# Optimization experiments

Measured on AMD Instinct MI355X. Metric: run time of the kernel, lower is better.

The kernel has to match this reference:

```python
import jax, jax.numpy as jnp
import numpy as np

B, C_IN, C_HID, H, W = 4, 512, 512, 64, 64


def setup_inputs() -> dict:
    key = jax.random.key(0)
    ks = jax.random.split(key, 9)
    s_in = 1.0 / np.sqrt(C_IN)
    s_hid = 1.0 / np.sqrt(C_HID)
    return {
        "inp": jax.random.normal(ks[0], (B, C_IN, H, W), dtype=jnp.float32),
        "Wk": jax.random.normal(ks[1], (C_HID, C_IN), dtype=jnp.float32) * s_in,
        "bk": jax.random.normal(ks[2], (C_HID,), dtype=jnp.float32) * 0.01,
        "Wq": jax.random.normal(ks[3], (C_HID, C_IN), dtype=jnp.float32) * s_in,
        "bq": jax.random.normal(ks[4], (C_HID,), dtype=jnp.float32) * 0.01,
        "Wv": jax.random.normal(ks[5], (C_HID, C_IN), dtype=jnp.float32) * s_in,
        "bv": jax.random.normal(ks[6], (C_HID,), dtype=jnp.float32) * 0.01,
        "Wo": jax.random.normal(ks[7], (C_IN, C_HID), dtype=jnp.float32) * s_hid,
        "bo": jax.random.normal(ks[8], (C_IN,), dtype=jnp.float32) * 0.01,
    }


def reference(inp, Wk, bk, Wq, bq, Wv, bv, Wo, bo):
    b, _, h, w = inp.shape
    n = h * w

    def conv1x1(x, Wt, bias):  # 1x1 conv == per-pixel GEMM
        return jnp.einsum('bchw,oc->bohw', x, Wt) + bias[None, :, None, None]

    k = conv1x1(inp, Wk, bk).reshape(b, C_HID, n)   # [B,Ch,N]
    q = conv1x1(inp, Wq, bq).reshape(b, C_HID, n)
    v = conv1x1(inp, Wv, bv).reshape(b, C_HID, n)

    scale = 1.0 / jnp.sqrt(jnp.asarray(C_HID, dtype=jnp.float32))
    # weight[b,i,j] = <key_i, query_j> / sqrt(Ch); softmax over j (dim=2)
    scores = jnp.einsum('bci,bcj->bij', k, q) * scale  # [B,N,N]
    weight = jax.nn.softmax(scores, axis=2)
    # out[b,c,i] = sum_j weight[b,i,j] * v[b,c,j]
    out = jnp.einsum('bij,bcj->bci', weight, v).reshape(b, C_HID, h, w)
    return conv1x1(out, Wo, bo)  # [B,C_in,H,W]
```

## Files before the change

### kernel.cpp

```cpp
#include <hip/hip_runtime.h>
#include <hip/hip_bf16.h>


typedef __attribute__((ext_vector_type(4))) float f32x4;
typedef __attribute__((ext_vector_type(8))) short short8;
typedef __attribute__((ext_vector_type(4))) short short4v;

#define QSCALE 0.06376639774f

__device__ __forceinline__ unsigned short f2bf(float f) {
  unsigned u = __builtin_bit_cast(unsigned, f);
  unsigned r = (u + 0x7FFFu + ((u >> 16) & 1u)) >> 16;
  return (unsigned short)r;
}

__device__ __forceinline__ void gll16(const void* g, void* l) {
  __builtin_amdgcn_global_load_lds((const __attribute__((address_space(1))) void*)g,
                                   (__attribute__((address_space(3))) void*)l, 16, 0, 0);
}

#define MFMA_BF16(d, va, vb) \
  d = __builtin_amdgcn_mfma_f32_16x16x32_bf16(va, vb, d, 0, 0, 0)

__device__ __forceinline__ void gemm_fat(
    const short* __restrict__ A, int lda,
    const short* __restrict__ B, int ldb,
    int nkt, char* sm, f32x4 (&acc)[8][4]) {
  const int tid = threadIdx.x, w = tid >> 6, lane = tid & 63;
  const int g = lane >> 4, l15 = lane & 15;
  const int swz = (l15 & 7) << 4;

  for (int t = 0; t < nkt; ++t) {
    __syncthreads();
#pragma unroll
    for (int reg = 0; reg < 3; ++reg) {
      const short* src = reg ? B : A;
      const int ld = reg ? ldb : lda;
      const int rbase = (reg == 2) ? 128 : 0;
#pragma unroll
      for (int pass = 0; pass < 4; ++pass) {
        int chunk = pass * 4 + w;
        int o = chunk * 1024 + lane * 16;
        int row = o >> 7;
        int cb = (o & 127) ^ ((row & 7) << 4);
        gll16((const char*)src + (size_t)(rbase + row) * (ld * 2) +
                  (size_t)t * 128 + cb,
              sm + reg * 16384 + chunk * 1024);
      }
    }
    __syncthreads();
#pragma unroll
    for (int ks = 0; ks < 2; ++ks) {
      short8 a[8], bb[4];
#pragma unroll
      for (int i = 0; i < 8; ++i)
        a[i] = *(const short8*)(sm + (i * 16 + l15) * 128 + ((ks * 64 + g * 16) ^ swz));
#pragma unroll
      for (int nf = 0; nf < 4; ++nf) {
        int r = w * 64 + nf * 16 + l15;
        bb[nf] = *(const short8*)(sm + 16384 + (r >> 7) * 16384 + (r & 127) * 128 +
                                  ((ks * 64 + g * 16) ^ swz));
      }
      __builtin_amdgcn_s_setprio(1);
#pragma unroll
      for (int i = 0; i < 8; ++i)
#pragma unroll
        for (int nf = 0; nf < 4; ++nf)
          MFMA_BF16(acc[i][nf], a[i], bb[nf]);
      __builtin_amdgcn_s_setprio(0);
    }
  }
}

__global__ __launch_bounds__(256) void cvt_w_kernel(
    const float* __restrict__ wk, const float* __restrict__ wq,
    const float* __restrict__ wv, const float* __restrict__ wo,
    short* __restrict__ o) {
  int z = blockIdx.y;
  const float* s = (z == 0) ? wk : (z == 1) ? wq : (z == 2) ? wv : wo;
  int i = blockIdx.x * 256 + threadIdx.x;
  float4 f = ((const float4*)s)[i];
  short4v v;
  v[0] = (short)f2bf(f.x); v[1] = (short)f2bf(f.y);
  v[2] = (short)f2bf(f.z); v[3] = (short)f2bf(f.w);
  if (z < 3) {
    *(short4v*)(o + z * 262144 + i * 4) = v;
  } else {
    int idx = i * 4, co = idx >> 9, cc = idx & 511;
    short* base = o + 786432 + co * 1024 + cc;
    *(short4v*)base = v;
    *(short4v*)(base + 512) = v;
  }
}

__global__ __launch_bounds__(256) void transpose_x_kernel(
    const float* __restrict__ inp, short* __restrict__ xt) {
  __shared__ float t[32][33];
  int tx = threadIdx.x, ty = threadIdx.y;
  int n0 = blockIdx.x * 32, c0 = blockIdx.y * 32, b = blockIdx.z;
  const float* src = inp + ((size_t)(b * 512 + c0)) * 4096 + n0;
#pragma unroll
  for (int r = 0; r < 4; ++r) t[ty + r * 8][tx] = src[(ty + r * 8) * 4096 + tx];
  __syncthreads();
  short* dst = xt + ((size_t)((b << 12) + n0)) * 512 + c0;
#pragma unroll
  for (int r = 0; r < 4; ++r) dst[(ty + r * 8) * 512 + tx] = (short)f2bf(t[tx][ty + r * 8]);
}

__global__ __launch_bounds__(256, 2) void kqv_kernel(
    const short* __restrict__ xt,
    const short* __restrict__ wk, const short* __restrict__ wq, const short* __restrict__ wv,
    const float* __restrict__ bk, const float* __restrict__ bq, const float* __restrict__ bv,
    short* __restrict__ kt, short* __restrict__ qt, short* __restrict__ vc) {
  __shared__ char sm[49152];
  const int bid = blockIdx.x;
  const int xcd = bid & 7, s = bid >> 3;
  const int gg = (s / 12) * 8 + xcd;
  const int t = s % 12;
  const int z = (t < 8) ? (t >> 2) : 2;
  const short *A, *B;
  int arow0, brow0;
  if (z < 2) {
    arow0 = gg * 256 + ((t >> 1) & 1) * 128;
    brow0 = (t & 1) * 256;
    A = xt + (size_t)arow0 * 512;
    B = ((z == 0) ? wk : wq) + (size_t)brow0 * 512;
  } else {
    arow0 = (t - 8) * 128;
    brow0 = gg * 256;
    A = wv + (size_t)arow0 * 512;
    B = xt + (size_t)brow0 * 512;
  }
  f32x4 acc[8][4] = {};
  gemm_fat(A, 512, B, 512, 8, sm, acc);
  const int tid = threadIdx.x, w = tid >> 6, lane = tid & 63;
  const int gq = lane >> 4, l15 = lane & 15;
#pragma unroll
  for (int mf = 0; mf < 8; ++mf)
#pragma unroll
    for (int nf = 0; nf < 4; ++nf)
#pragma unroll
      for (int r = 0; r < 4; ++r) {
        int row = mf * 16 + gq * 4 + r;
        int col = w * 64 + nf * 16 + l15;
        float v = acc[mf][nf][r];
        if (z == 0)      kt[(size_t)(arow0 + row) * 512 + brow0 + col] =
                           (short)f2bf((v + bk[brow0 + col]) * QSCALE);
        else if (z == 1) qt[(size_t)(arow0 + row) * 512 + brow0 + col] =
                           (short)f2bf(v + bq[brow0 + col]);
        else             vc[(size_t)(arow0 + row) * 16384 + brow0 + col] =
                           (short)f2bf(v + bv[arow0 + row]);
      }
}

__global__ __launch_bounds__(256, 2) void gemm_s_kernel(
    const short* __restrict__ kt, const short* __restrict__ qt,
    short* __restrict__ P, float* __restrict__ Lpart) {
  __shared__ char sm[49152];
  const int bid = blockIdx.x;
  const int xcd = bid & 7, s = bid >> 3;
  const int b = xcd >> 1, h = xcd & 1;
  const int it = s >> 3, jt = s & 7;
  const int i0 = it * 128, jt0 = jt * 256;
  const short* A = kt + ((size_t)((b << 12) + i0)) * 512;
  const short* B = qt + ((size_t)((b << 12) + h * 2048 + jt0)) * 512;
  f32x4 acc[8][4] = {};
  gemm_fat(A, 512, B, 512, 8, sm, acc);
  const int tid = threadIdx.x, w = tid >> 6, lane = tid & 63;
  const int gq = lane >> 4, l15 = lane & 15;
  short* Pb = P + (size_t)h * 33554432 + ((size_t)((b << 12) + i0)) * 2048 + jt0;
  float psum[8][4];
#pragma unroll
  for (int mf = 0; mf < 8; ++mf)
#pragma unroll
    for (int r = 0; r < 4; ++r) psum[mf][r] = 0.f;
#pragma unroll
  for (int mf = 0; mf < 8; ++mf)
#pragma unroll
    for (int nf = 0; nf < 4; ++nf)
#pragma unroll
      for (int r = 0; r < 4; ++r) {
        float p = exp2f(acc[mf][nf][r]);
        psum[mf][r] += p;
        int row = mf * 16 + gq * 4 + r;
        int col = w * 64 + nf * 16 + l15;
        Pb[(size_t)row * 2048 + col] = (short)f2bf(p);
      }
  const int jp = (h * 2048 + jt0 + w * 64) >> 6;
  float* Lp = Lpart + (((size_t)b * 64 + jp) << 12) + i0;
#pragma unroll
  for (int mf = 0; mf < 8; ++mf)
#pragma unroll
    for (int r = 0; r < 4; ++r) {
      float ss = psum[mf][r];
      ss += __shfl_xor(ss, 1); ss += __shfl_xor(ss, 2);
      ss += __shfl_xor(ss, 4); ss += __shfl_xor(ss, 8);
      if (l15 == 0) Lp[mf * 16 + gq * 4 + r] = ss;
    }
}

__global__ __launch_bounds__(256, 2) void gemm_pv_kernel(
    const short* __restrict__ P, const short* __restrict__ vc,
    short* __restrict__ otab) {
  __shared__ char sm[49152];
  const int bid = blockIdx.x;
  const int xcd = bid & 7, s = bid >> 3;
  const int b = xcd >> 1, h = xcd & 1;
  const int it = s >> 1, ct = s & 1;
  const int i0 = it * 128, c0 = ct * 256;
  const short* A = P + (size_t)h * 33554432 + ((size_t)((b << 12) + i0)) * 2048;
  const short* B = vc + (size_t)c0 * 16384 + (b << 12) + h * 2048;
  f32x4 acc[8][4] = {};
  gemm_fat(A, 2048, B, 16384, 32, sm, acc);
  const int tid = threadIdx.x, w = tid >> 6, lane = tid & 63;
  const int gq = lane >> 4, l15 = lane & 15;
  short* Ob = otab + ((size_t)((b << 12) + i0)) * 1024 + h * 512 + c0;
#pragma unroll
  for (int mf = 0; mf < 8; ++mf)
#pragma unroll
    for (int nf = 0; nf < 4; ++nf)
#pragma unroll
      for (int r = 0; r < 4; ++r) {
        int row = mf * 16 + gq * 4 + r;
        int col = w * 64 + nf * 16 + l15;
        Ob[(size_t)row * 1024 + col] = (short)f2bf(acc[mf][nf][r]);
      }
}

__global__ __launch_bounds__(256) void lred_kernel(
    const float* __restrict__ Lpart, float* __restrict__ linv) {
  int i = blockIdx.x * 256 + threadIdx.x;
  int b = i >> 12;
  float s = 0.f;
#pragma unroll 8
  for (int jp = 0; jp < 64; ++jp) s += Lpart[(((size_t)b * 64 + jp) << 12) + (i & 4095)];
  linv[i] = 1.0f / s;
}

__global__ __launch_bounds__(256, 2) void gemm_out_kernel(
    const short* __restrict__ wdup, const short* __restrict__ otab,
    const float* __restrict__ bo, const float* __restrict__ linv,
    float* __restrict__ out) {
  __shared__ char sm[49152];
  const int bid = blockIdx.x;
  const int xcd = bid & 7, s = bid >> 3;
  const int b = xcd >> 1, ch = xcd & 1;
  const int cot = ch * 2 + (s & 1);
  const int nt = s >> 1;
  const int arow0 = cot * 128;
  const int bn0 = nt * 256;
  const short* A = wdup + (size_t)arow0 * 1024;
  const short* B = otab + ((size_t)((b << 12) + bn0)) * 1024;
  f32x4 acc[8][4] = {};
  gemm_fat(A, 1024, B, 1024, 16, sm, acc);
  const int tid = threadIdx.x, w = tid >> 6, lane = tid & 63;
  const int gq = lane >> 4, l15 = lane & 15;
#pragma unroll
  for (int mf = 0; mf < 8; ++mf) {
    int co = arow0 + mf * 16 + gq * 4;
#pragma unroll
    for (int nf = 0; nf < 4; ++nf) {
      int nl = bn0 + w * 64 + nf * 16 + l15;
      float li = linv[(b << 12) + nl];
#pragma unroll
      for (int r = 0; r < 4; ++r)
        out[((size_t)(b * 512 + co + r) << 12) + nl] = acc[mf][nf][r] * li + bo[co + r];
    }
  }
}

extern "C" void kernel_launch(void* const* d_in, const int* in_sizes, int n_in,
                              void* d_out, int out_size, void* d_ws, size_t ws_size,
                              hipStream_t stream) {
  const float* inp = (const float*)d_in[0];
  const float* Wk = (const float*)d_in[1];
  const float* bk = (const float*)d_in[2];
  const float* Wq = (const float*)d_in[3];
  const float* bq = (const float*)d_in[4];
  const float* Wv = (const float*)d_in[5];
  const float* bv = (const float*)d_in[6];
  const float* Wo = (const float*)d_in[7];
  const float* bo = (const float*)d_in[8];
  float* out = (float*)d_out;
  char* ws = (char*)d_ws;
  const size_t MB = 1048576;
  short* kt    = (short*)(ws);
  short* qt    = (short*)(ws + 16 * MB);
  short* vc    = (short*)(ws + 32 * MB);
  short* wb    = (short*)(ws + 48 * MB);
  short* xt    = (short*)(ws + 51 * MB);
  float* Lpart = (float*)(ws + 51 * MB);
  float* linv  = (float*)(ws + 55 * MB);
  short* P     = (short*)(ws + 67 * MB);
  short* otab  = (short*)(ws + 195 * MB);

  (void)in_sizes; (void)n_in; (void)out_size; (void)ws_size;

  cvt_w_kernel<<<dim3(256, 4), 256, 0, stream>>>(Wk, Wq, Wv, Wo, wb);
  transpose_x_kernel<<<dim3(128, 16, 4), dim3(32, 8, 1), 0, stream>>>(inp, xt);
  kqv_kernel<<<768, 256, 0, stream>>>(
      xt, wb, wb + 262144, wb + 524288, bk, bq, bv, kt, qt, vc);
  gemm_s_kernel<<<2048, 256, 0, stream>>>(kt, qt, P, Lpart);
  gemm_pv_kernel<<<512, 256, 0, stream>>>(P, vc, otab);
  lred_kernel<<<64, 256, 0, stream>>>(Lpart, linv);
  gemm_out_kernel<<<256, 256, 0, stream>>>(wb + 786432, otab, bo, linv, out);
}
```

Before: 274.7 us.

## Quantize K and Q to int8 for the score GEMM and switch to fp16

Moves all bf16 storage and MFMA math to fp16. K and Q are now quantized to int8 with per-row absmax scales in a new quant kernel, so the score GEMM can use i32 16x16x64 int8 MFMA over half the K-tiles and half the bytes. Dequantization multiplies in the row and column scales, and a fixed exponent offset of -4 keeps fp16 P within range. The aim is to cut the cost of the score GEMM. It adds an extra quantization pass and int8 rounding error in the attention scores, which may affect accuracy.

New measurement: 266.8 us. -2.9%, faster.

```diff
diff --git a/kernel.cpp b/kernel.cpp
--- a/kernel.cpp
+++ b/kernel.cpp
@@ -3,15 +3,16 @@
 
 
 typedef __attribute__((ext_vector_type(4))) float f32x4;
-typedef __attribute__((ext_vector_type(8))) short short8;
+typedef __attribute__((ext_vector_type(4))) int i32x4;
+typedef _Float16 half8 __attribute__((ext_vector_type(8)));
 typedef __attribute__((ext_vector_type(4))) short short4v;
-
-#define QSCALE 0.06376639774f
-
-__device__ __forceinline__ unsigned short f2bf(float f) {
-  unsigned u = __builtin_bit_cast(unsigned, f);
-  unsigned r = (u + 0x7FFFu + ((u >> 16) & 1u)) >> 16;
-  return (unsigned short)r;
+typedef __attribute__((ext_vector_type(8))) signed char schar8;
+
+#define SQRT_QS 0.2525200f
+
+__device__ __forceinline__ unsigned short f2h(float f) {
+  _Float16 h = (_Float16)f;
+  return __builtin_bit_cast(unsigned short, h);
 }
 
 __device__ __forceinline__ void gll16(const void* g, void* l) {
@@ -19,8 +20,10 @@
                                    (__attribute__((address_space(3))) void*)l, 16, 0, 0);
 }
 
-#define MFMA_BF16(d, va, vb) \
-  d = __builtin_amdgcn_mfma_f32_16x16x32_bf16(va, vb, d, 0, 0, 0)
+#define MFMA_F16(d, va, vb) \
+  d = __builtin_amdgcn_mfma_f32_16x16x32_f16(va, vb, d, 0, 0, 0)
+#define MFMA_I8(d, va, vb) \
+  d = __builtin_amdgcn_mfma_i32_16x16x64_i8(va, vb, d, 0, 0, 0)
 
 __device__ __forceinline__ void gemm_fat(
     const short* __restrict__ A, int lda,
@@ -51,22 +54,71 @@
     __syncthreads();
 #pragma unroll
     for (int ks = 0; ks < 2; ++ks) {
-      short8 a[8], bb[4];
+      half8 a[8], bb[4];
 #pragma unroll
       for (int i = 0; i < 8; ++i)
-        a[i] = *(const short8*)(sm + (i * 16 + l15) * 128 + ((ks * 64 + g * 16) ^ swz));
+        a[i] = *(const half8*)(sm + (i * 16 + l15) * 128 + ((ks * 64 + g * 16) ^ swz));
 #pragma unroll
       for (int nf = 0; nf < 4; ++nf) {
         int r = w * 64 + nf * 16 + l15;
-        bb[nf] = *(const short8*)(sm + 16384 + (r >> 7) * 16384 + (r & 127) * 128 +
-                                  ((ks * 64 + g * 16) ^ swz));
+        bb[nf] = *(const half8*)(sm + 16384 + (r >> 7) * 16384 + (r & 127) * 128 +
+                                 ((ks * 64 + g * 16) ^ swz));
       }
       __builtin_amdgcn_s_setprio(1);
 #pragma unroll
       for (int i = 0; i < 8; ++i)
 #pragma unroll
         for (int nf = 0; nf < 4; ++nf)
-          MFMA_BF16(acc[i][nf], a[i], bb[nf]);
+          MFMA_F16(acc[i][nf], a[i], bb[nf]);
+      __builtin_amdgcn_s_setprio(0);
+    }
+  }
+}
+
+__device__ __forceinline__ void gemm_fat_i8(
+    const signed char* __restrict__ A, int ldaB,
+    const signed char* __restrict__ B, int ldbB,
+    int nkt, char* sm, i32x4 (&acc)[8][4]) {
+  const int tid = threadIdx.x, w = tid >> 6, lane = tid & 63;
+  const int g = lane >> 4, l15 = lane & 15;
+  const int swz = (l15 & 7) << 4;
+
+  for (int t = 0; t < nkt; ++t) {
+    __syncthreads();
+#pragma unroll
+    for (int reg = 0; reg < 3; ++reg) {
+      const signed char* src = reg ? B : A;
+      const int ld = reg ? ldbB : ldaB;
+      const int rbase = (reg == 2) ? 128 : 0;
+#pragma unroll
+      for (int pass = 0; pass < 4; ++pass) {
+        int chunk = pass * 4 + w;
+        int o = chunk * 1024 + lane * 16;
+        int row = o >> 7;
+        int cb = (o & 127) ^ ((row & 7) << 4);
+        gll16((const char*)src + (size_t)(rbase + row) * ld + (size_t)t * 128 + cb,
+              sm + reg * 16384 + chunk * 1024);
+      }
+    }
+    __syncthreads();
+#pragma unroll
+    for (int ks = 0; ks < 2; ++ks) {
+      i32x4 a[8], bb[4];
+#pragma unroll
+      for (int i = 0; i < 8; ++i)
+        a[i] = *(const i32x4*)(sm + (i * 16 + l15) * 128 + ((ks * 64 + g * 16) ^ swz));
+#pragma unroll
+      for (int nf = 0; nf < 4; ++nf) {
+        int r = w * 64 + nf * 16 + l15;
+        bb[nf] = *(const i32x4*)(sm + 16384 + (r >> 7) * 16384 + (r & 127) * 128 +
+                                 ((ks * 64 + g * 16) ^ swz));
+      }
+      __builtin_amdgcn_s_setprio(1);
+#pragma unroll
+      for (int i = 0; i < 8; ++i)
+#pragma unroll
+        for (int nf = 0; nf < 4; ++nf)
+          MFMA_I8(acc[i][nf], a[i], bb[nf]);
       __builtin_amdgcn_s_setprio(0);
     }
   }
@@ -81,8 +133,8 @@
   int i = blockIdx.x * 256 + threadIdx.x;
   float4 f = ((const float4*)s)[i];
   short4v v;
-  v[0] = (short)f2bf(f.x); v[1] = (short)f2bf(f.y);
-  v[2] = (short)f2bf(f.z); v[3] = (short)f2bf(f.w);
+  v[0] = (short)f2h(f.x); v[1] = (short)f2h(f.y);
+  v[2] = (short)f2h(f.z); v[3] = (short)f2h(f.w);
   if (z < 3) {
     *(short4v*)(o + z * 262144 + i * 4) = v;
   } else {
@@ -104,14 +156,15 @@
   __syncthreads();
   short* dst = xt + ((size_t)((b << 12) + n0)) * 512 + c0;
 #pragma unroll
-  for (int r = 0; r < 4; ++r) dst[(ty + r * 8) * 512 + tx] = (short)f2bf(t[tx][ty + r * 8]);
+  for (int r = 0; r < 4; ++r) dst[(ty + r * 8) * 512 + tx] = (short)f2h(t[tx][ty + r * 8]);
 }
 
 __global__ __launch_bounds__(256, 2) void kqv_kernel(
     const short* __restrict__ xt,
     const short* __restrict__ wk, const short* __restrict__ wq, const short* __restrict__ wv,
     const float* __restrict__ bk, const float* __restrict__ bq, const float* __restrict__ bv,
-    short* __restrict__ kt, short* __restrict__ qt, short* __restrict__ vc) {
+    short* __restrict__ kth, short* __restrict__ qth,
+    short* __restrict__ vc) {
   __shared__ char sm[49152];
   const int bid = blockIdx.x;
   const int xcd = bid & 7, s = bid >> 3;
@@ -144,17 +197,41 @@
         int row = mf * 16 + gq * 4 + r;
         int col = w * 64 + nf * 16 + l15;
         float v = acc[mf][nf][r];
-        if (z == 0)      kt[(size_t)(arow0 + row) * 512 + brow0 + col] =
-                           (short)f2bf((v + bk[brow0 + col]) * QSCALE);
-        else if (z == 1) qt[(size_t)(arow0 + row) * 512 + brow0 + col] =
-                           (short)f2bf(v + bq[brow0 + col]);
-        else             vc[(size_t)(arow0 + row) * 16384 + brow0 + col] =
-                           (short)f2bf(v + bv[arow0 + row]);
-      }
+        if (z == 2) {
+          vc[(size_t)(arow0 + row) * 16384 + brow0 + col] =
+              (short)f2h(v + bv[arow0 + row]);
+        } else {
+          short* dst = (z == 0) ? kth : qth;
+          float bias = (z == 0) ? bk[brow0 + col] : bq[brow0 + col];
+          dst[(size_t)(arow0 + row) * 512 + brow0 + col] = (short)f2h(v + bias);
+        }
+      }
+}
+
+__global__ __launch_bounds__(256) void quant_kernel(
+    const short* __restrict__ src, signed char* __restrict__ dst,
+    float* __restrict__ scl) {
+  const int row = blockIdx.x * 4 + (threadIdx.x >> 6);
+  const int lane = threadIdx.x & 63;
+  half8 v = *(const half8*)(src + (size_t)row * 512 + lane * 8);
+  float f[8];
+  float m = 0.f;
+#pragma unroll
+  for (int e = 0; e < 8; ++e) { f[e] = (float)v[e]; m = fmaxf(m, fabsf(f[e])); }
+#pragma unroll
+  for (int off = 1; off < 64; off <<= 1) m = fmaxf(m, __shfl_xor(m, off));
+  m = fmaxf(m, 1e-6f);
+  const float inv = 127.0f / m;
+  schar8 q;
+#pragma unroll
+  for (int e = 0; e < 8; ++e) q[e] = (signed char)(int)rintf(f[e] * inv);
+  *(schar8*)(dst + (size_t)row * 512 + lane * 8) = q;
+  if (lane == 0) scl[row] = m * (SQRT_QS / 127.0f);
 }
 
 __global__ __launch_bounds__(256, 2) void gemm_s_kernel(
-    const short* __restrict__ kt, const short* __restrict__ qt,
+    const signed char* __restrict__ kt8, const signed char* __restrict__ qt8,
+    const float* __restrict__ sk, const float* __restrict__ sq,
     short* __restrict__ P, float* __restrict__ Lpart) {
   __shared__ char sm[49152];
   const int bid = blockIdx.x;
@@ -162,12 +239,17 @@
   const int b = xcd >> 1, h = xcd & 1;
   const int it = s >> 3, jt = s & 7;
   const int i0 = it * 128, jt0 = jt * 256;
-  const short* A = kt + ((size_t)((b << 12) + i0)) * 512;
-  const short* B = qt + ((size_t)((b << 12) + h * 2048 + jt0)) * 512;
-  f32x4 acc[8][4] = {};
-  gemm_fat(A, 512, B, 512, 8, sm, acc);
+  const signed char* A = kt8 + ((size_t)((b << 12) + i0)) * 512;
+  const signed char* B = qt8 + ((size_t)((b << 12) + h * 2048 + jt0)) * 512;
+  i32x4 acc[8][4] = {};
+  gemm_fat_i8(A, 512, B, 512, 4, sm, acc);
   const int tid = threadIdx.x, w = tid >> 6, lane = tid & 63;
   const int gq = lane >> 4, l15 = lane & 15;
+  const float* skp = sk + (b << 12) + i0;
+  const float* sqp = sq + (b << 12) + h * 2048 + jt0;
+  float sqc[4];
+#pragma unroll
+  for (int nf = 0; nf < 4; ++nf) sqc[nf] = sqp[w * 64 + nf * 16 + l15];
   short* Pb = P + (size_t)h * 33554432 + ((size_t)((b << 12) + i0)) * 2048 + jt0;
   float psum[8][4];
 #pragma unroll
@@ -175,17 +257,21 @@
 #pragma unroll
     for (int r = 0; r < 4; ++r) psum[mf][r] = 0.f;
 #pragma unroll
-  for (int mf = 0; mf < 8; ++mf)
+  for (int mf = 0; mf < 8; ++mf) {
+    float skr[4];
+#pragma unroll
+    for (int r = 0; r < 4; ++r) skr[r] = skp[mf * 16 + gq * 4 + r];
 #pragma unroll
     for (int nf = 0; nf < 4; ++nf)
 #pragma unroll
       for (int r = 0; r < 4; ++r) {
-        float p = exp2f(acc[mf][nf][r]);
+        float p = exp2f((float)acc[mf][nf][r] * skr[r] * sqc[nf] - 4.0f);
         psum[mf][r] += p;
         int row = mf * 16 + gq * 4 + r;
         int col = w * 64 + nf * 16 + l15;
-        Pb[(size_t)row * 2048 + col] = (short)f2bf(p);
-      }
+        Pb[(size_t)row * 2048 + col] = (short)f2h(p);
+      }
+  }
   const int jp = (h * 2048 + jt0 + w * 64) >> 6;
   float* Lp = Lpart + (((size_t)b * 64 + jp) << 12) + i0;
 #pragma unroll
@@ -223,7 +309,7 @@
       for (int r = 0; r < 4; ++r) {
         int row = mf * 16 + gq * 4 + r;
         int col = w * 64 + nf * 16 + l15;
-        Ob[(size_t)row * 1024 + col] = (short)f2bf(acc[mf][nf][r]);
+        Ob[(size_t)row * 1024 + col] = (short)f2h(acc[mf][nf][r]);
       }
 }
 
@@ -284,14 +370,17 @@
   float* out = (float*)d_out;
   char* ws = (char*)d_ws;
   const size_t MB = 1048576;
-  short* kt    = (short*)(ws);
-  short* qt    = (short*)(ws + 16 * MB);
+  signed char* kt8 = (signed char*)(ws);
+  signed char* qt8 = (signed char*)(ws + 8 * MB);
+  float* sk    = (float*)(ws + 16 * MB);
   short* vc    = (short*)(ws + 32 * MB);
   short* wb    = (short*)(ws + 48 * MB);
   short* xt    = (short*)(ws + 51 * MB);
   float* Lpart = (float*)(ws + 51 * MB);
   float* linv  = (float*)(ws + 55 * MB);
   short* P     = (short*)(ws + 67 * MB);
+  short* kth   = (short*)(ws + 67 * MB);
+  short* qth   = (short*)(ws + 83 * MB);
   short* otab  = (short*)(ws + 195 * MB);
 
   (void)in_sizes; (void)n_in; (void)out_size; (void)ws_size;
@@ -299,8 +388,10 @@
   cvt_w_kernel<<<dim3(256, 4), 256, 0, stream>>>(Wk, Wq, Wv, Wo, wb);
   transpose_x_kernel<<<dim3(128, 16, 4), dim3(32, 8, 1), 0, stream>>>(inp, xt);
   kqv_kernel<<<768, 256, 0, stream>>>(
-      xt, wb, wb + 262144, wb + 524288, bk, bq, bv, kt, qt, vc);
-  gemm_s_kernel<<<2048, 256, 0, stream>>>(kt, qt, P, Lpart);
+      xt, wb, wb + 262144, wb + 524288, bk, bq, bv, kth, qth, vc);
+  quant_kernel<<<8192, 256, 0, stream>>>(kth, kt8, sk);
+  gemm_s_kernel<<<2048, 256, 0, stream>>>(
+      kt8, qt8, sk, sk + 16384, P, Lpart);
   gemm_pv_kernel<<<512, 256, 0, stream>>>(P, vc, otab);
   lred_kernel<<<64, 256, 0, stream>>>(Lpart, linv);
   gemm_out_kernel<<<256, 256, 0, stream>>>(wb + 786432, otab, bo, linv, out);
```
